# Optimization experiments

Hardware: AMD Instinct MI355X
Metric: run time of the kernel (lower is better)

Reference implementation:

```python
import jax, jax.numpy as jnp
import numpy as np

C = 1.5          # Poincare ball curvature (geoopt PoincareBallExact(c=1.5))
TEMP = 0.1       # logits temperature
EPS = 1e-5       # artanh clamp, matches geoopt fp32 eps


def _mlp(x, w1, b1, w2, b2, w3, b3):
    # torch nn.GELU default is the exact erf formulation
    h = jax.nn.gelu(x @ w1 + b1, approximate=False)
    h = jax.nn.gelu(h @ w2 + b2, approximate=False)
    return h @ w3 + b3


def _expmap0(u):
    # geoopt expmap0: tanh(sqrt(c)*||u||) * u / (sqrt(c)*||u||)
    sqrt_c = jnp.sqrt(C)
    n = jnp.maximum(jnp.linalg.norm(u, axis=-1, keepdims=True), 1e-15)
    return jnp.tanh(sqrt_c * n) * u / (sqrt_c * n)


def _poincare_dist(protos, y):
    """Pairwise Poincare distance. protos: (P, d) on-ball, y: (B, d) on-ball -> (B, P).
    dist(x, y) = 2/sqrt(c) * artanh(sqrt(c) * ||mobius_add(-x, y)||)
    """
    sqrt_c = jnp.sqrt(C)
    x = -protos                               # (P, d)
    x2 = jnp.sum(x * x, axis=-1)              # (P,)
    y2 = jnp.sum(y * y, axis=-1)              # (B,)
    xy = y @ x.T                              # (B, P) = <x, y> broadcast
    a = 1.0 + 2.0 * C * xy + C * y2[:, None]  # coeff of x
    b = 1.0 - C * x2[None, :]                 # coeff of y
    denom = 1.0 + 2.0 * C * xy + (C * C) * x2[None, :] * y2[:, None]
    denom = jnp.maximum(jnp.abs(denom), 1e-15)
    # only one (B, P, d) intermediate: the mobius-add numerator
    num = a[:, :, None] * x[None, :, :] + b[:, :, None] * y[:, None, :]
    r = sqrt_c * jnp.linalg.norm(num, axis=-1) / denom   # (B, P)
    r = jnp.clip(r, 0.0, 1.0 - EPS)
    return (2.0 / sqrt_c) * jnp.arctanh(r)


def setup_inputs() -> dict:
    key = jax.random.key(0)
    ks = jax.random.split(key, 16)
    B, DIN, H, D = 64, 768, 4096, 256
    PG, PS = 500, 5000

    def lin(kw, kb, fan_in, fan_out):
        s = 1.0 / np.sqrt(fan_in)
        w = jax.random.uniform(kw, (fan_in, fan_out), jnp.float32, -s, s)
        b = jax.random.uniform(kb, (fan_out,), jnp.float32, -s, s)
        return w, b

    x = jax.random.normal(ks[0], (B, DIN), jnp.float32)
    # prototypes: random points well inside the ball (radius 1/sqrt(1.5) ~ 0.816)
    protos_genus = 0.01 * jax.random.normal(ks[1], (PG, D), jnp.float32)
    protos_species = 0.01 * jax.random.normal(ks[2], (PS, D), jnp.float32)

    w1g, b1g = lin(ks[3], ks[4], DIN, H)
    w2g, b2g = lin(ks[5], ks[6], H, H)
    w3g, b3g = lin(ks[7], ks[8], H, D)
    w1s, b1s = lin(ks[9], ks[10], DIN, H)
    w2s, b2s = lin(ks[11], ks[12], H, H)
    w3s, b3s = lin(ks[13], ks[14], H, D)

    return {
        "x": x, "protos_genus": protos_genus, "protos_species": protos_species,
        "w1g": w1g, "b1g": b1g, "w2g": w2g, "b2g": b2g, "w3g": w3g, "b3g": b3g,
        "w1s": w1s, "b1s": b1s, "w2s": w2s, "b2s": b2s, "w3s": w3s, "b3s": b3s,
    }


def reference(x, protos_genus, protos_species,
              w1g, b1g, w2g, b2g, w3g, b3g,
              w1s, b1s, w2s, b2s, w3s, b3s):
    feat_g = _mlp(x, w1g, b1g, w2g, b2g, w3g, b3g)   # (B, D) euclidean
    feat_s = _mlp(x, w1s, b1s, w2s, b2s, w3s, b3s)
    hyp_g = _expmap0(feat_g)
    hyp_s = _expmap0(feat_s)
    logits_g = -_poincare_dist(protos_genus, hyp_g) / TEMP    # (B, PG)
    logits_s = -_poincare_dist(protos_species, hyp_s) / TEMP  # (B, PS)
    return (logits_g, logits_s)
```

## Files before the change

kernel.cpp:

```cpp
#include <hip/hip_runtime.h>
#include <hip/hip_bf16.h>
#include <math.h>

typedef unsigned short ushort_t;
typedef unsigned int uint_t;

#define C_CURV 1.5f
#define SQRT_C 1.22474487139158905f
#define TEMP_ 0.1f

typedef __attribute__((ext_vector_type(8))) short short8;
typedef __attribute__((ext_vector_type(4))) float f32x4;

static __device__ __forceinline__ ushort_t f2bf(float f) {
  union { float f; uint_t u; } v; v.f = f;
  uint_t u = v.u;
  uint_t r = (u + 0x7FFFu + ((u >> 16) & 1u)) >> 16;
  return (ushort_t)r;
}

static __device__ __forceinline__ float b2f(ushort_t h) {
  union { uint_t u; float f; } v; v.u = ((uint_t)h) << 16;
  return v.f;
}

static __device__ __forceinline__ float gelu_exact(float x) {
  return 0.5f * x * (1.0f + erff(x * 0.70710678118654752f));
}

#define GLOAD_LDS16(gp, lp) __builtin_amdgcn_global_load_lds( \
    (const __attribute__((address_space(1))) void*)(const void*)(gp), \
    (__attribute__((address_space(3))) void*)(void*)(lp), 16, 0, 0)

__global__ void k_cvt_x(const float* __restrict__ x, ushort_t* __restrict__ xb, int n4) {
  int i = blockIdx.x * blockDim.x + threadIdx.x;
  if (i >= n4) return;
  float4 v = reinterpret_cast<const float4*>(x)[i];
  ushort4 o;
  o.x = f2bf(v.x); o.y = f2bf(v.y); o.z = f2bf(v.z); o.w = f2bf(v.w);
  reinterpret_cast<ushort4*>(xb)[i] = o;
}

__global__ __launch_bounds__(256) void k_gemm(
    const ushort_t* __restrict__ Abase, long a_br_stride,
    const float* __restrict__ Wg, const float* __restrict__ Ws,
    ushort_t* __restrict__ partial, int N, int K, int kchunk)
{
  __shared__ float    sW[4][32][256];
  __shared__ ushort_t sA[4][64][32];

  const int tn = blockIdx.x, ks = blockIdx.y, br = blockIdx.z;
  const int KS = gridDim.y;
  const ushort_t* A = Abase + (long)br * a_br_stride;
  const float* W = br ? Ws : Wg;
  const int lane = threadIdx.x & 63;
  const int w = threadIdx.x >> 6;
  const int c = lane & 15;
  const int g = lane >> 4;
  const int n0b = tn * 256;
  const int k0 = ks * kchunk;

  const float* wst = W + (long)(k0 + w * 8) * N + n0b + lane * 4;
  const ushort_t* ast = A + (long)(w * 16 + (lane >> 2)) * K + k0 + (lane & 3) * 8;

  f32x4 acc[4][4];
  #pragma unroll
  for (int mi = 0; mi < 4; ++mi)
    #pragma unroll
    for (int nf = 0; nf < 4; ++nf) acc[mi][nf] = f32x4{0.f, 0.f, 0.f, 0.f};

#define STAGE(buf, t) do { \
    _Pragma("unroll") for (int i = 0; i < 8; ++i) \
      GLOAD_LDS16(wst + (long)((t) * 32 + i) * N, &sW[buf][w * 8 + i][0]); \
    GLOAD_LDS16(ast + (t) * 32, &sA[buf][w * 16][0]); \
  } while (0)

#define COMPUTE(buf) do { \
    short8 af[4]; \
    _Pragma("unroll") for (int mi = 0; mi < 4; ++mi) \
      af[mi] = *reinterpret_cast<const short8*>(&sA[buf][c + 16 * mi][8 * g]); \
    _Pragma("unroll") for (int nf = 0; nf < 4; ++nf) { \
      float bw[8]; \
      _Pragma("unroll") for (int j = 0; j < 8; ++j) \
        bw[j] = sW[buf][8 * g + j][w * 64 + nf * 16 + c]; \
      short8 bf; \
      _Pragma("unroll") for (int j = 0; j < 8; ++j) bf[j] = (short)f2bf(bw[j]); \
      _Pragma("unroll") for (int mi = 0; mi < 4; ++mi) \
        acc[mi][nf] = __builtin_amdgcn_mfma_f32_16x16x32_bf16(af[mi], bf, acc[mi][nf], 0, 0, 0); \
    } \
  } while (0)

  const int nt = kchunk >> 5;
  STAGE(0, 0);
  STAGE(1, 1);
  STAGE(2, 2);
  int t = 0;
  for (; t + 3 < nt; ++t) {
    asm volatile("s_waitcnt vmcnt(18)" ::: "memory");
    __builtin_amdgcn_s_barrier();
    STAGE((t + 3) & 3, t + 3);
    COMPUTE(t & 3);
  }
  asm volatile("s_waitcnt vmcnt(18)" ::: "memory");
  __builtin_amdgcn_s_barrier();
  COMPUTE(t & 3); ++t;
  asm volatile("s_waitcnt vmcnt(9)" ::: "memory");
  __builtin_amdgcn_s_barrier();
  COMPUTE(t & 3); ++t;
  asm volatile("s_waitcnt vmcnt(0)" ::: "memory");
  __builtin_amdgcn_s_barrier();
  COMPUTE(t & 3);
#undef STAGE
#undef COMPUTE

  ushort_t* po = partial + (long)(br * KS + ks) * 64 * N;
  #pragma unroll
  for (int mi = 0; mi < 4; ++mi)
    #pragma unroll
    for (int nf = 0; nf < 4; ++nf)
      #pragma unroll
      for (int q = 0; q < 4; ++q) {
        int b = 16 * mi + 4 * g + q;
        po[(long)b * N + n0b + w * 64 + nf * 16 + c] = f2bf(acc[mi][nf][q]);
      }
}

__global__ void k_reduce_gelu(const ushort_t* __restrict__ partial,
    const float* __restrict__ bg, const float* __restrict__ bs,
    ushort_t* __restrict__ hb, int N, int KS, int total8)
{
  int i = blockIdx.x * blockDim.x + threadIdx.x;
  if (i >= total8) return;
  int perbr8 = 64 * N / 8;
  int br = i / perbr8;
  int rem = i - br * perbr8;
  const short8* pp = reinterpret_cast<const short8*>(partial) + (long)br * KS * perbr8 + rem;
  float s[8] = {0.f, 0.f, 0.f, 0.f, 0.f, 0.f, 0.f, 0.f};
  for (int ks = 0; ks < KS; ++ks) {
    short8 t = pp[(long)ks * perbr8];
    #pragma unroll
    for (int j = 0; j < 8; ++j) s[j] += b2f((ushort_t)t[j]);
  }
  int n8 = rem % (N / 8);
  float4 bv0 = reinterpret_cast<const float4*>(br ? bs : bg)[n8 * 2];
  float4 bv1 = reinterpret_cast<const float4*>(br ? bs : bg)[n8 * 2 + 1];
  s[0] += bv0.x; s[1] += bv0.y; s[2] += bv0.z; s[3] += bv0.w;
  s[4] += bv1.x; s[5] += bv1.y; s[6] += bv1.z; s[7] += bv1.w;
  short8 o;
  #pragma unroll
  for (int j = 0; j < 8; ++j) o[j] = (short)f2bf(gelu_exact(s[j]));
  reinterpret_cast<short8*>(hb)[i] = o;
}

__global__ __launch_bounds__(256) void k_expmap(const ushort_t* __restrict__ partial,
    const float* __restrict__ b3g, const float* __restrict__ b3s,
    ushort_t* __restrict__ hypb, float* __restrict__ y2, int KS)
{
  int b = blockIdx.x, br = blockIdx.y, d = threadIdx.x;
  const ushort_t* pp = partial + (long)(br * KS) * 64 * 256 + (long)b * 256 + d;
  float s = 0.f;
  #pragma unroll 8
  for (int ks = 0; ks < KS; ++ks) s += b2f(pp[(long)ks * 64 * 256]);
  s += (br ? b3s : b3g)[d];

  float v = s * s;
  #pragma unroll
  for (int off = 1; off < 64; off <<= 1) v += __shfl_xor(v, off);
  __shared__ float red[4];
  __shared__ float n2s;
  if ((threadIdx.x & 63) == 0) red[threadIdx.x >> 6] = v;
  __syncthreads();
  if (threadIdx.x == 0) n2s = red[0] + red[1] + red[2] + red[3];
  __syncthreads();
  float n = fmaxf(sqrtf(n2s), 1e-15f);
  float sn = SQRT_C * n;
  float t = tanhf(sn);
  float scale = t / sn;
  hypb[((long)br * 64 + b) * 256 + d] = f2bf(s * scale);
  if (threadIdx.x == 0) y2[br * 64 + b] = t * t / C_CURV;
}

__global__ __launch_bounds__(256) void k_dist(const float* __restrict__ pg,
    const float* __restrict__ ps, const ushort_t* __restrict__ hypb,
    const float* __restrict__ y2, float* __restrict__ out)
{
  int u = blockIdx.x * 4 + (threadIdx.x >> 6);
  const int lane = threadIdx.x & 63;
  const int c = lane & 15, g = lane >> 4;
  const float* protos; const ushort_t* A; const float* y2p; float* ob; int P;
  if (u < 128) {
    protos = pg; P = 500; A = hypb; y2p = y2; ob = out;
  } else {
    u -= 128;
    if (u >= 1252) return;
    protos = ps; P = 5000; A = hypb + 64 * 256; y2p = y2 + 64; ob = out + 64 * 500;
  }
  const int w = u >> 2;
  const int mi = u & 3;
  int p = w * 16 + c;
  int pc = min(p, P - 1);
  const float* pp = protos + (long)pc * 256 + 8 * g;
  const ushort_t* ap = A + (long)(c + 16 * mi) * 256 + 8 * g;

  f32x4 acc = {0.f, 0.f, 0.f, 0.f};
  float x2p = 0.f;

  #pragma unroll
  for (int s8 = 0; s8 < 8; ++s8) {
    float4 v0 = *reinterpret_cast<const float4*>(pp + 32 * s8);
    float4 v1 = *reinterpret_cast<const float4*>(pp + 32 * s8 + 4);
    x2p += v0.x * v0.x + v0.y * v0.y + v0.z * v0.z + v0.w * v0.w
         + v1.x * v1.x + v1.y * v1.y + v1.z * v1.z + v1.w * v1.w;
    short8 bfr;
    bfr[0] = (short)f2bf(v0.x); bfr[1] = (short)f2bf(v0.y);
    bfr[2] = (short)f2bf(v0.z); bfr[3] = (short)f2bf(v0.w);
    bfr[4] = (short)f2bf(v1.x); bfr[5] = (short)f2bf(v1.y);
    bfr[6] = (short)f2bf(v1.z); bfr[7] = (short)f2bf(v1.w);
    short8 af = *reinterpret_cast<const short8*>(ap + 32 * s8);
    acc = __builtin_amdgcn_mfma_f32_16x16x32_bf16(af, bfr, acc, 0, 0, 0);
  }
  x2p += __shfl_xor(x2p, 16);
  x2p += __shfl_xor(x2p, 32);
  const float x2 = x2p;
  const float bb = 1.f - C_CURV * x2;
  const float LC = -2.f / (SQRT_C * TEMP_);

  if (p < P) {
    #pragma unroll
    for (int q = 0; q < 4; ++q) {
      int b = 16 * mi + 4 * g + q;
      float xy = -acc[q];
      float y2v = y2p[b];
      float a = 1.f + 2.f * C_CURV * xy + C_CURV * y2v;
      float den = fabsf(1.f + 2.f * C_CURV * xy + C_CURV * C_CURV * x2 * y2v);
      den = fmaxf(den, 1e-15f);
      float num2 = a * a * x2 + 2.f * a * bb * xy + bb * bb * y2v;
      num2 = fmaxf(num2, 0.f);
      float r = SQRT_C * sqrtf(num2) / den;
      r = fminf(r, 1.f - 1e-5f);
      r = fmaxf(r, 0.f);
      ob[(long)b * P + p] = LC * atanhf(r);
    }
  }
}

extern "C" void kernel_launch(void* const* d_in, const int* in_sizes, int n_in,
                              void* d_out, int out_size, void* d_ws, size_t ws_size,
                              hipStream_t stream) {
  const float* x   = (const float*)d_in[0];
  const float* pg  = (const float*)d_in[1];
  const float* ps  = (const float*)d_in[2];
  const float* w1g = (const float*)d_in[3];
  const float* b1g = (const float*)d_in[4];
  const float* w2g = (const float*)d_in[5];
  const float* b2g = (const float*)d_in[6];
  const float* w3g = (const float*)d_in[7];
  const float* b3g = (const float*)d_in[8];
  const float* w1s = (const float*)d_in[9];
  const float* b1s = (const float*)d_in[10];
  const float* w2s = (const float*)d_in[11];
  const float* b2s = (const float*)d_in[12];
  const float* w3s = (const float*)d_in[13];
  const float* b3s = (const float*)d_in[14];
  float* out = (float*)d_out;
  char* ws = (char*)d_ws;
  (void)in_sizes; (void)n_in; (void)out_size; (void)ws_size;

  const int KS1 = 6, KS2 = 8, KS3 = 32;
  size_t PART = (size_t)KS2 * 2 * 64 * 4096 * 2;

  ushort_t* partial = (ushort_t*)(ws);
  ushort_t* xb      = (ushort_t*)(ws + PART);
  ushort_t* h1b     = (ushort_t*)(ws + PART + 98304);
  ushort_t* h2b     = (ushort_t*)(ws + PART + 98304 + 1048576);
  ushort_t* hypb    = (ushort_t*)(ws + PART + 98304 + 2097152);
  float*    y2      = (float*)   (ws + PART + 98304 + 2097152 + 65536);

  k_cvt_x<<<48, 256, 0, stream>>>(x, xb, 64 * 768 / 4);
  k_gemm<<<dim3(16, KS1, 2), 256, 0, stream>>>(xb, 0L, w1g, w1s, partial, 4096, 768, 768 / KS1);
  k_reduce_gelu<<<256, 256, 0, stream>>>(partial, b1g, b1s, h1b, 4096, KS1, 2 * 64 * 4096 / 8);
  k_gemm<<<dim3(16, KS2, 2), 256, 0, stream>>>(h1b, (long)64 * 4096, w2g, w2s, partial, 4096, 4096, 4096 / KS2);
  k_reduce_gelu<<<256, 256, 0, stream>>>(partial, b2g, b2s, h2b, 4096, KS2, 2 * 64 * 4096 / 8);
  k_gemm<<<dim3(1, KS3, 2), 256, 0, stream>>>(h2b, (long)64 * 4096, w3g, w3s, partial, 256, 4096, 4096 / KS3);
  k_expmap<<<dim3(64, 2), 256, 0, stream>>>(partial, b3g, b3s, hypb, y2, KS3);
  k_dist<<<345, 256, 0, stream>>>(pg, ps, hypb, y2, out);
}
```

Baseline: 85.09 us.

## Shrink GEMM tile to 128 columns with 8 waves and triple buffering

The split-K GEMM now uses 512-thread blocks that each cover 128 output columns. Each wave computes a single 16-column fragment instead of four, so accumulators drop from 16 to 4 vectors. LDS buffering drops from four stages to three, and only the first four waves load the activation tile. This cuts registers and LDS per block so more blocks fit on a CU, and it doubles the grid for better latency hiding. The cost is that each fp32 weight element loaded into LDS now feeds only 4 MFMAs instead of 16, and there is less pipelining depth. KS1 is also raised from 6 to 8.

```diff
diff --git a/kernel.cpp b/kernel.cpp
--- a/kernel.cpp
+++ b/kernel.cpp
@@ -41,13 +41,13 @@
   reinterpret_cast<ushort4*>(xb)[i] = o;
 }
 
-__global__ __launch_bounds__(256) void k_gemm(
+__global__ __launch_bounds__(512, 4) void k_gemm(
     const ushort_t* __restrict__ Abase, long a_br_stride,
     const float* __restrict__ Wg, const float* __restrict__ Ws,
     ushort_t* __restrict__ partial, int N, int K, int kchunk)
 {
-  __shared__ float    sW[4][32][256];
-  __shared__ ushort_t sA[4][64][32];
+  __shared__ float    sW[3][32][128];
+  __shared__ ushort_t sA[3][64][32];
 
   const int tn = blockIdx.x, ks = blockIdx.y, br = blockIdx.z;
   const int KS = gridDim.y;
@@ -57,72 +57,62 @@
   const int w = threadIdx.x >> 6;
   const int c = lane & 15;
   const int g = lane >> 4;
-  const int n0b = tn * 256;
+  const int n0b = tn * 128;
   const int k0 = ks * kchunk;
-
-  const float* wst = W + (long)(k0 + w * 8) * N + n0b + lane * 4;
+  const bool hasA = (w < 4);
+
+  const float* wst = W + (long)(k0 + w * 4 + (lane >> 5)) * N + n0b + (lane & 31) * 4;
   const ushort_t* ast = A + (long)(w * 16 + (lane >> 2)) * K + k0 + (lane & 3) * 8;
 
-  f32x4 acc[4][4];
-  #pragma unroll
-  for (int mi = 0; mi < 4; ++mi)
-    #pragma unroll
-    for (int nf = 0; nf < 4; ++nf) acc[mi][nf] = f32x4{0.f, 0.f, 0.f, 0.f};
+  f32x4 acc[4];
+  #pragma unroll
+  for (int mi = 0; mi < 4; ++mi) acc[mi] = f32x4{0.f, 0.f, 0.f, 0.f};
 
 #define STAGE(buf, t) do { \
-    _Pragma("unroll") for (int i = 0; i < 8; ++i) \
-      GLOAD_LDS16(wst + (long)((t) * 32 + i) * N, &sW[buf][w * 8 + i][0]); \
-    GLOAD_LDS16(ast + (t) * 32, &sA[buf][w * 16][0]); \
+    GLOAD_LDS16(wst + (long)((t) * 32) * N,     &sW[buf][w * 4][0]); \
+    GLOAD_LDS16(wst + (long)((t) * 32 + 2) * N, &sW[buf][w * 4 + 2][0]); \
+    if (hasA) GLOAD_LDS16(ast + (t) * 32, &sA[buf][w * 16][0]); \
   } while (0)
 
 #define COMPUTE(buf) do { \
     short8 af[4]; \
     _Pragma("unroll") for (int mi = 0; mi < 4; ++mi) \
       af[mi] = *reinterpret_cast<const short8*>(&sA[buf][c + 16 * mi][8 * g]); \
-    _Pragma("unroll") for (int nf = 0; nf < 4; ++nf) { \
-      float bw[8]; \
-      _Pragma("unroll") for (int j = 0; j < 8; ++j) \
-        bw[j] = sW[buf][8 * g + j][w * 64 + nf * 16 + c]; \
-      short8 bf; \
-      _Pragma("unroll") for (int j = 0; j < 8; ++j) bf[j] = (short)f2bf(bw[j]); \
-      _Pragma("unroll") for (int mi = 0; mi < 4; ++mi) \
-        acc[mi][nf] = __builtin_amdgcn_mfma_f32_16x16x32_bf16(af[mi], bf, acc[mi][nf], 0, 0, 0); \
-    } \
+    float bw[8]; \
+    _Pragma("unroll") for (int j = 0; j < 8; ++j) \
+      bw[j] = sW[buf][8 * g + j][w * 16 + c]; \
+    short8 bf; \
+    _Pragma("unroll") for (int j = 0; j < 8; ++j) bf[j] = (short)f2bf(bw[j]); \
+    _Pragma("unroll") for (int mi = 0; mi < 4; ++mi) \
+      acc[mi] = __builtin_amdgcn_mfma_f32_16x16x32_bf16(af[mi], bf, acc[mi], 0, 0, 0); \
   } while (0)
 
   const int nt = kchunk >> 5;
   STAGE(0, 0);
   STAGE(1, 1);
-  STAGE(2, 2);
   int t = 0;
-  for (; t + 3 < nt; ++t) {
-    asm volatile("s_waitcnt vmcnt(18)" ::: "memory");
+  for (; t < nt - 1; ++t) {
+    if (hasA) asm volatile("s_waitcnt vmcnt(3)" ::: "memory");
+    else      asm volatile("s_waitcnt vmcnt(2)" ::: "memory");
     __builtin_amdgcn_s_barrier();
-    STAGE((t + 3) & 3, t + 3);
-    COMPUTE(t & 3);
-  }
-  asm volatile("s_waitcnt vmcnt(18)" ::: "memory");
-  __builtin_amdgcn_s_barrier();
-  COMPUTE(t & 3); ++t;
-  asm volatile("s_waitcnt vmcnt(9)" ::: "memory");
-  __builtin_amdgcn_s_barrier();
-  COMPUTE(t & 3); ++t;
+    if (t + 2 < nt) STAGE((t + 2) % 3, t + 2);
+    COMPUTE(t % 3);
+  }
   asm volatile("s_waitcnt vmcnt(0)" ::: "memory");
   __builtin_amdgcn_s_barrier();
-  COMPUTE(t & 3);
+  COMPUTE(t % 3);
 #undef STAGE
 #undef COMPUTE
 
   ushort_t* po = partial + (long)(br * KS + ks) * 64 * N;
+  const int n0 = n0b + w * 16 + c;
   #pragma unroll
   for (int mi = 0; mi < 4; ++mi)
     #pragma unroll
-    for (int nf = 0; nf < 4; ++nf)
-      #pragma unroll
-      for (int q = 0; q < 4; ++q) {
-        int b = 16 * mi + 4 * g + q;
-        po[(long)b * N + n0b + w * 64 + nf * 16 + c] = f2bf(acc[mi][nf][q]);
-      }
+    for (int q = 0; q < 4; ++q) {
+      int b = 16 * mi + 4 * g + q;
+      po[(long)b * N + n0] = f2bf(acc[mi][q]);
+    }
 }
 
 __global__ void k_reduce_gelu(const ushort_t* __restrict__ partial,
@@ -266,7 +256,7 @@
   char* ws = (char*)d_ws;
   (void)in_sizes; (void)n_in; (void)out_size; (void)ws_size;
 
-  const int KS1 = 6, KS2 = 8, KS3 = 32;
+  const int KS1 = 8, KS2 = 8, KS3 = 32;
   size_t PART = (size_t)KS2 * 2 * 64 * 4096 * 2;
 
   ushort_t* partial = (ushort_t*)(ws);
@@ -277,11 +267,11 @@
   float*    y2      = (float*)   (ws + PART + 98304 + 2097152 + 65536);
 
   k_cvt_x<<<48, 256, 0, stream>>>(x, xb, 64 * 768 / 4);
-  k_gemm<<<dim3(16, KS1, 2), 256, 0, stream>>>(xb, 0L, w1g, w1s, partial, 4096, 768, 768 / KS1);
+  k_gemm<<<dim3(32, KS1, 2), 512, 0, stream>>>(xb, 0L, w1g, w1s, partial, 4096, 768, 768 / KS1);
   k_reduce_gelu<<<256, 256, 0, stream>>>(partial, b1g, b1s, h1b, 4096, KS1, 2 * 64 * 4096 / 8);
-  k_gemm<<<dim3(16, KS2, 2), 256, 0, stream>>>(h1b, (long)64 * 4096, w2g, w2s, partial, 4096, 4096, 4096 / KS2);
+  k_gemm<<<dim3(32, KS2, 2), 512, 0, stream>>>(h1b, (long)64 * 4096, w2g, w2s, partial, 4096, 4096, 4096 / KS2);
   k_reduce_gelu<<<256, 256, 0, stream>>>(partial, b2g, b2s, h2b, 4096, KS2, 2 * 64 * 4096 / 8);
-  k_gemm<<<dim3(1, KS3, 2), 256, 0, stream>>>(h2b, (long)64 * 4096, w3g, w3s, partial, 256, 4096, 4096 / KS3);
+  k_gemm<<<dim3(2, KS3, 2), 512, 0, stream>>>(h2b, (long)64 * 4096, w3g, w3s, partial, 256, 4096, 4096 / KS3);
   k_expmap<<<dim3(64, 2), 256, 0, stream>>>(partial, b3g, b3s, hypb, y2, KS3);
   k_dist<<<345, 256, 0, stream>>>(pg, ps, hypb, y2, out);
 }
```

After: 71.62 us. -15.8%, faster.
